# Kernel optimization log

Measured on AMD Instinct MI355X. Metric: run time of the kernel, lower is better.

## Reference

```python
import jax, jax.numpy as jnp
import numpy as np

DIM = 512
H = 48
W = 48
WS = 6
NH = 16
HEAD = DIM // NH
SCALE = HEAD ** -0.5
MLP_RATIO = 4
EPS = 1e-3  # keras LayerNormalization default epsilon
B = 16
L = H * W
M = WS * WS
NW = (H // WS) * (W // WS)


def _rel_pos_index(ws):
    # replicates tf.meshgrid (indexing='xy') construction exactly
    ch = np.arange(ws)
    cw = np.arange(ws)
    coords = np.stack(np.meshgrid(ch, cw))              # (2, ws, ws)
    cf = coords.reshape(2, -1)                          # (2, M)
    cf1 = np.concatenate([cf, np.zeros((2, 1), cf.dtype)], axis=1)  # (2, M+1) with global (0,0)
    rel = cf[:, :, None] - cf1[:, None, :]              # (2, M, M+1)
    rel = rel.transpose(1, 2, 0).copy()
    rel[:, :, 0] += ws - 1
    rel[:, :, 1] += ws - 1
    rel[:, :, 0] *= 2 * ws - 1
    return rel.sum(-1)                                  # (M, M+1)

REL_IDX = jnp.asarray(_rel_pos_index(WS))


def layernorm(x, g, b):
    m = x.mean(-1, keepdims=True)
    v = ((x - m) ** 2).mean(-1, keepdims=True)
    return (x - m) / jnp.sqrt(v + EPS) * g + b


def setup_inputs() -> dict:
    key = jax.random.key(0)
    ks = jax.random.split(key, 8)
    dense = lambda k, i, o: jax.random.normal(k, (i, o), jnp.float32) * (1.0 / np.sqrt(i))
    return dict(
        x=jax.random.normal(ks[0], (B, L, DIM), jnp.float32),
        xavg=jax.random.normal(ks[1], (B, 1, DIM), jnp.float32),
        w_kv=dense(ks[2], DIM, 2 * DIM), b_kv=jnp.zeros((2 * DIM,), jnp.float32),
        w_q=dense(ks[3], DIM, DIM), b_q=jnp.zeros((DIM,), jnp.float32),
        rel_bias_table=jax.random.normal(ks[4], ((2 * WS - 1) ** 2, NH), jnp.float32) * 0.02,
        g1=jnp.ones((DIM,), jnp.float32), be1=jnp.zeros((DIM,), jnp.float32),
        g2=jnp.ones((DIM,), jnp.float32), be2=jnp.zeros((DIM,), jnp.float32),
        w_fc1=dense(ks[5], DIM, MLP_RATIO * DIM), b_fc1=jnp.zeros((MLP_RATIO * DIM,), jnp.float32),
        w_fc2=dense(ks[6], MLP_RATIO * DIM, DIM), b_fc2=jnp.zeros((DIM,), jnp.float32),
    )


def _heads(t):
    # (B*, N, C) -> (B*, NH, N, HEAD)
    return t.reshape(t.shape[0], t.shape[1], NH, HEAD).transpose(0, 2, 1, 3)


def _forward(x, xavg, w_kv, b_kv, w_q, b_q, rel_bias_table, g1, be1, g2, be2,
             w_fc1, b_fc1, w_fc2, b_fc2):
    shortcut, shortcut_avg = x, xavg
    xn = layernorm(x, g1, be1)                          # (B, L, C)
    xavgn = layernorm(xavg, g1, be1)                    # (B, 1, C)

    # window partition: (B, L, C) -> (B*NW, M, C)
    xw = xn.reshape(B, H // WS, WS, W // WS, WS, DIM)
    xw = xw.transpose(0, 1, 3, 2, 4, 5).reshape(B * NW, M, DIM)

    # per-window tokens + repeated global token as keys/values
    xavgR = jnp.repeat(xavgn, NW, axis=0)               # (B*NW, 1, C), batch-major like tf.repeat
    x_c = jnp.concatenate([xw, xavgR], axis=1)          # (B*NW, M+1, C)

    kv = x_c @ w_kv + b_kv                              # (B*NW, M+1, 2C)
    q = xw @ w_q + b_q                                  # (B*NW, M, C)
    q_avg = xavgn @ w_q + b_q                           # (B, 1, C)
    kv_g = xn @ w_kv + b_kv                             # (B, L, 2C)

    k, v = jnp.split(kv, 2, axis=-1)
    kg, vg = jnp.split(kv_g, 2, axis=-1)

    qh = _heads(q) * SCALE                              # (B*NW, NH, M, HEAD)
    attn = jnp.einsum('bhqd,bhkd->bhqk', qh, _heads(k))  # (B*NW, NH, M, M+1)
    bias = rel_bias_table[REL_IDX.reshape(-1)].reshape(M, M + 1, NH)
    attn = attn + bias.transpose(2, 0, 1)[None]
    attn = jax.nn.softmax(attn, axis=-1)
    xo = jnp.einsum('bhqk,bhkd->bhqd', attn, _heads(v))
    xo = xo.transpose(0, 2, 1, 3).reshape(B * NW, M, DIM)

    # global token attends to all tokens
    qg = _heads(q_avg) * SCALE                          # (B, NH, 1, HEAD)
    attng = jax.nn.softmax(jnp.einsum('bhqd,bhkd->bhqk', qg, _heads(kg)), axis=-1)
    xavg_o = jnp.einsum('bhqk,bhkd->bhqd', attng, _heads(vg))
    xavg_o = xavg_o.transpose(0, 2, 1, 3).reshape(B, 1, DIM)

    # window reverse: (B*NW, M, C) -> (B, L, C)
    xr = xo.reshape(B, H // WS, W // WS, WS, WS, DIM)
    xr = xr.transpose(0, 1, 3, 2, 4, 5).reshape(B, L, DIM)

    x = shortcut + xr
    xavg = shortcut_avg + xavg_o

    mlp = lambda t: jax.nn.gelu(t @ w_fc1 + b_fc1, approximate=False) @ w_fc2 + b_fc2
    x = x + mlp(layernorm(x, g2, be2))
    xavg = xavg + mlp(layernorm(xavg, g2, be2))
    return x, xavg


def reference(x, xavg, w_kv, b_kv, w_q, b_q, rel_bias_table, g1, be1, g2, be2,
              w_fc1, b_fc1, w_fc2, b_fc2):
    return _forward(x, xavg, w_kv, b_kv, w_q, b_q, rel_bias_table, g1, be1, g2, be2,
                    w_fc1, b_fc1, w_fc2, b_fc2)
```

## Files before the change

kernel.cpp:

```cpp
#include <hip/hip_runtime.h>
#include <stdint.h>

#define DIM 512
#define NHEAD 16
#define HEADD 32
#define BATCH 16
#define SEQL 2304
#define XROWS (BATCH*SEQL)
#define NROWS (XROWS + BATCH)
#define ATT_SCALE 0.17677669529663687f

typedef __attribute__((ext_vector_type(8))) short short8;
typedef __attribute__((ext_vector_type(4))) float f32x4;

__device__ __forceinline__ float bf2f(unsigned short v) {
    union { unsigned u; float f; } t; t.u = ((unsigned)v) << 16; return t.f;
}
__device__ __forceinline__ unsigned short f2bf(float f) {
    union { float f; unsigned u; } t; t.f = f;
    unsigned r = t.u + 0x7fffu + ((t.u >> 16) & 1u);
    return (unsigned short)(r >> 16);
}
__device__ __forceinline__ void unpack8(const int4 c, float* o) {
    union { unsigned u; float f; } t;
    unsigned w0 = (unsigned)c.x, w1 = (unsigned)c.y, w2 = (unsigned)c.z, w3 = (unsigned)c.w;
    t.u = w0 << 16;         o[0] = t.f;
    t.u = w0 & 0xffff0000u; o[1] = t.f;
    t.u = w1 << 16;         o[2] = t.f;
    t.u = w1 & 0xffff0000u; o[3] = t.f;
    t.u = w2 << 16;         o[4] = t.f;
    t.u = w2 & 0xffff0000u; o[5] = t.f;
    t.u = w3 << 16;         o[6] = t.f;
    t.u = w3 & 0xffff0000u; o[7] = t.f;
}
__device__ __forceinline__ void gl_lds16(const void* g, void* l) {
    __builtin_amdgcn_global_load_lds((const __attribute__((address_space(1))) unsigned int*)g,
                                     (__attribute__((address_space(3))) unsigned int*)l,
                                     16, 0, 0);
}

__device__ __forceinline__ float gelu_exact(float v) {
    union { float f; unsigned u; } zc; zc.f = v * 0.70710678118654752f;
    unsigned sgn = zc.u & 0x80000000u;
    union { float f; unsigned u; } az; az.u = zc.u & 0x7fffffffu;
    float t  = __builtin_amdgcn_rcpf(fmaf(0.3275911f, az.f, 1.0f));
    float p  = t * fmaf(t, fmaf(t, fmaf(t, fmaf(t, 1.061405429f, -1.453152027f),
                                        1.421413741f), -0.284496736f), 0.254829592f);
    float e  = __expf(-az.f * az.f);
    union { float f; unsigned u; } er; er.f = fmaf(-p, e, 1.0f);
    er.u |= sgn;
    return 0.5f * v * (1.0f + er.f);
}

__device__ __forceinline__ void ln_row(const float* __restrict__ src, int lane,
                                       const float* __restrict__ g, const float* __restrict__ be,
                                       unsigned short* __restrict__ outrow) {
    int c0 = lane * 8;
    float4 v0 = *(const float4*)(src + c0);
    float4 v1 = *(const float4*)(src + c0 + 4);
    float s = v0.x+v0.y+v0.z+v0.w + v1.x+v1.y+v1.z+v1.w;
    float q = v0.x*v0.x+v0.y*v0.y+v0.z*v0.z+v0.w*v0.w + v1.x*v1.x+v1.y*v1.y+v1.z*v1.z+v1.w*v1.w;
    for (int m = 1; m < 64; m <<= 1) { s += __shfl_xor(s, m); q += __shfl_xor(q, m); }
    float mean = s * (1.0f/512.0f);
    float var  = q * (1.0f/512.0f) - mean*mean;
    float rs = rsqrtf(var + 1e-3f);
    float4 g0 = *(const float4*)(g + c0);
    float4 g1 = *(const float4*)(g + c0 + 4);
    float4 b0 = *(const float4*)(be + c0);
    float4 b1 = *(const float4*)(be + c0 + 4);
    unsigned short o[8];
    o[0] = f2bf((v0.x-mean)*rs*g0.x + b0.x);
    o[1] = f2bf((v0.y-mean)*rs*g0.y + b0.y);
    o[2] = f2bf((v0.z-mean)*rs*g0.z + b0.z);
    o[3] = f2bf((v0.w-mean)*rs*g0.w + b0.w);
    o[4] = f2bf((v1.x-mean)*rs*g1.x + b1.x);
    o[5] = f2bf((v1.y-mean)*rs*g1.y + b1.y);
    o[6] = f2bf((v1.z-mean)*rs*g1.z + b1.z);
    o[7] = f2bf((v1.w-mean)*rs*g1.w + b1.w);
    *(int4*)(outrow + c0) = *(const int4*)o;
}

#define TPOSE_BLKS 2816
#define SPACK_BLKS 90
#define LN1_BLKS   9220
__global__ __launch_bounds__(256) void prep_kernel(const float* __restrict__ w_q,
                                                   const float* __restrict__ w_kv,
                                                   const float* __restrict__ w_fc1,
                                                   const float* __restrict__ w_fc2,
                                                   unsigned short* __restrict__ Wqkv_t,
                                                   unsigned short* __restrict__ Wfc1_t,
                                                   unsigned short* __restrict__ Wfc2_t,
                                                   const float* __restrict__ b_q,
                                                   const float* __restrict__ b_kv,
                                                   const float* __restrict__ rel_table,
                                                   float* __restrict__ bqkv,
                                                   float* __restrict__ bias_exp,
                                                   const float* __restrict__ x,
                                                   const float* __restrict__ xavg,
                                                   const float* __restrict__ g1,
                                                   const float* __restrict__ be1,
                                                   unsigned short* __restrict__ xn) {
    __shared__ float tile[32][33];
    int blk = blockIdx.x;
    if (blk < TPOSE_BLKS) {
        int t = blk;
        const float* src; unsigned short* dst;
        int Kd, Nd, rowOff, tk;
        if (t < 256)        { src = w_q;   dst = Wqkv_t; Kd = 512;  Nd = 512;  rowOff = 0;   tk = 16; }
        else if (t < 768)   { t -= 256;  src = w_kv;  dst = Wqkv_t; Kd = 512;  Nd = 1024; rowOff = 512; tk = 16; }
        else if (t < 1792)  { t -= 768;  src = w_fc1; dst = Wfc1_t; Kd = 512;  Nd = 2048; rowOff = 0;   tk = 16; }
        else                { t -= 1792; src = w_fc2; dst = Wfc2_t; Kd = 2048; Nd = 512;  rowOff = 0;   tk = 64; }
        int k0 = (t % tk) * 32;
        int n0 = (t / tk) * 32;
        int tx = threadIdx.x & 31, ty = threadIdx.x >> 5;
        #pragma unroll
        for (int r = 0; r < 32; r += 8)
            tile[r + ty][tx] = src[(long)(k0 + r + ty) * Nd + n0 + tx];
        __syncthreads();
        #pragma unroll
        for (int r = 0; r < 32; r += 8)
            dst[(long)(rowOff + n0 + r + ty) * Kd + k0 + tx] = f2bf(tile[tx][r + ty]);
        return;
    }
    blk -= TPOSE_BLKS;
    if (blk < SPACK_BLKS) {
        int i = blk * 256 + threadIdx.x;
        if (i < 1536) { bqkv[i] = (i < 512) ? b_q[i] : b_kv[i - 512]; return; }
        i -= 1536;
        if (i < NHEAD*36*37) {
            int h = i / (36*37); int rem = i % (36*37); int qi = rem / 37; int j = rem % 37;
            int c0m = qi % 6, c1m = qi / 6;
            int c0n = (j < 36) ? (j % 6) : 0;
            int c1n = (j < 36) ? (j / 6) : 0;
            int id = (c0m - c0n + 5) * 11 + (c1m - c1n + 5);
            bias_exp[i] = rel_table[id * NHEAD + h];
        }
        return;
    }
    blk -= SPACK_BLKS;
    int wv = threadIdx.x >> 6, lane = threadIdx.x & 63;
    int r = blk * 4 + wv;
    if (r >= NROWS) return;
    const float* src = (r < XROWS) ? (x + (long)r * DIM) : (xavg + (long)(r - XROWS) * DIM);
    ln_row(src, lane, g1, be1, xn + (long)r * DIM);
}

__global__ __launch_bounds__(256) void ln_kernel(const float* __restrict__ p1,
                                                 const float* __restrict__ g, const float* __restrict__ be,
                                                 unsigned short* __restrict__ out, int nrows) {
    int wv = threadIdx.x >> 6, lane = threadIdx.x & 63;
    int r = blockIdx.x * 4 + wv;
    if (r >= nrows) return;
    ln_row(p1 + (long)r * DIM, lane, g, be, out + (long)r * DIM);
}

template<bool GELU_ACT, bool OUT_BF16, bool HAS_RES>
__global__ __launch_bounds__(256) void gemm_kernel(const short* __restrict__ A,
                                                   const short* __restrict__ Bt,
                                                   const float* __restrict__ bias,
                                                   void* __restrict__ Cout,
                                                   const float* __restrict__ Res,
                                                   int M, int N, int K, int nbx) {
    __shared__ short lds_a[128 * 64];
    __shared__ short lds_b[128 * 64];
    const int tid = threadIdx.x;
    const int lane = tid & 63;
    const int wv = tid >> 6;

    const int nwg = gridDim.x;
    const int orig = blockIdx.x;
    const int q = nwg >> 3, r = nwg & 7;
    const int xcd = orig & 7, lid = orig >> 3;
    const int wg = (xcd < r ? xcd * (q + 1) : r * (q + 1) + (xcd - r) * q) + lid;
    const int m0 = (wg / nbx) * 128;
    const int n0 = (wg % nbx) * 128;
    const int wm = (wv >> 1) * 64;
    const int wn = (wv & 1) * 64;

    f32x4 acc[4][4];
    #pragma unroll
    for (int i = 0; i < 4; i++)
        #pragma unroll
        for (int j = 0; j < 4; j++) { acc[i][j][0]=0.f; acc[i][j][1]=0.f; acc[i][j][2]=0.f; acc[i][j][3]=0.f; }

    const int srow = tid >> 3;
    const int msl  = (tid & 7) ^ (srow & 7);
    const short* Aa = A + (long)(m0 + srow) * K + msl * 8;
    const short* Bb = Bt + (long)(n0 + srow) * K + msl * 8;
    short* la = lds_a + tid * 8;
    short* lb = lds_b + tid * 8;

    const int quad = lane >> 4;
    const int l15 = lane & 15;
    const short* ra0 = lds_a + (wm + l15) * 64 + ((quad)     ^ (l15 & 7)) * 8;
    const short* ra1 = lds_a + (wm + l15) * 64 + ((4 + quad) ^ (l15 & 7)) * 8;
    const short* rb0 = lds_b + (wn + l15) * 64 + ((quad)     ^ (l15 & 7)) * 8;
    const short* rb1 = lds_b + (wn + l15) * 64 + ((4 + quad) ^ (l15 & 7)) * 8;

    for (int k0 = 0; k0 < K; k0 += 64) {
        __syncthreads();
        #pragma unroll
        for (int i = 0; i < 4; i++) {
            gl_lds16(Aa + (long)(i * 32) * K + k0, la + i * 256 * 8);
            gl_lds16(Bb + (long)(i * 32) * K + k0, lb + i * 256 * 8);
        }
        __syncthreads();
        short8 af[4], bf4[4];
        #pragma unroll
        for (int mt = 0; mt < 4; mt++) af[mt] = *(const short8*)(ra0 + mt * 16 * 64);
        #pragma unroll
        for (int nt = 0; nt < 4; nt++) bf4[nt] = *(const short8*)(rb0 + nt * 16 * 64);
        #pragma unroll
        for (int mt = 0; mt < 4; mt++)
            #pragma unroll
            for (int nt = 0; nt < 4; nt++)
                acc[mt][nt] = __builtin_amdgcn_mfma_f32_16x16x32_bf16(af[mt], bf4[nt], acc[mt][nt], 0, 0, 0);
        #pragma unroll
        for (int mt = 0; mt < 4; mt++) af[mt] = *(const short8*)(ra1 + mt * 16 * 64);
        #pragma unroll
        for (int nt = 0; nt < 4; nt++) bf4[nt] = *(const short8*)(rb1 + nt * 16 * 64);
        #pragma unroll
        for (int mt = 0; mt < 4; mt++)
            #pragma unroll
            for (int nt = 0; nt < 4; nt++)
                acc[mt][nt] = __builtin_amdgcn_mfma_f32_16x16x32_bf16(af[mt], bf4[nt], acc[mt][nt], 0, 0, 0);
    }

    #pragma unroll
    for (int mt = 0; mt < 4; mt++) {
        int rbase = m0 + wm + mt * 16 + quad * 4;
        #pragma unroll
        for (int nt = 0; nt < 4; nt++) {
            int col = n0 + wn + nt * 16 + l15;
            float bv = bias[col];
            #pragma unroll
            for (int r2 = 0; r2 < 4; r2++) {
                int row = rbase + r2;
                if (row < M) {
                    float v = acc[mt][nt][r2] + bv;
                    if (GELU_ACT) v = gelu_exact(v);
                    if (HAS_RES) v += Res[(long)row * N + col];
                    if (OUT_BF16) ((unsigned short*)Cout)[(long)row * N + col] = f2bf(v);
                    else          ((float*)Cout)[(long)row * N + col] = v;
                }
            }
        }
    }
}

__global__ __launch_bounds__(256) void attn_kernel(const short* __restrict__ qkv,
                                                   const float* __restrict__ bias_exp,
                                                   const float* __restrict__ xin,
                                                   const float* __restrict__ xavg,
                                                   float* __restrict__ XALL) {
    __shared__ float kvs[4][37 * 64];
    const int tid = threadIdx.x;
    if (blockIdx.x < 4096) {
        const int wv = tid >> 6;
        const int lane = tid & 63;
        const int gw = blockIdx.x * 4 + wv;
        const int win = gw >> 4;
        const int h = gw & 15;
        const int b = win >> 6;
        const int i1 = (win >> 3) & 7;
        const int i3 = win & 7;

        float* lws = kvs[wv];

        for (int c = lane; c < 296; c += 64) {
            int cc = c;
            int voff = 512;
            int doff = 0;
            if (cc >= 148) { cc -= 148; voff = 1024; doff = 32; }
            int row = cc >> 2;
            int part = cc & 3;
            int grow;
            if (row < 36) { int i2 = row / 6, i4 = row % 6; grow = b * SEQL + (i1*6 + i2) * 48 + i3*6 + i4; }
            else grow = XROWS + b;
            int4 raw = *(const int4*)(qkv + (long)grow * 1536 + voff + h * 32 + part * 8);
            float tmp[8];
            unpack8(raw, tmp);
            float* dstp = &lws[row * 64 + doff + part * 8];
            *(float4*)dstp       = make_float4(tmp[0], tmp[1], tmp[2], tmp[3]);
            *(float4*)(dstp + 4) = make_float4(tmp[4], tmp[5], tmp[6], tmp[7]);
        }
        __syncthreads();

        const int qi = lane;
        if (qi >= 36) return;
        int i2 = qi / 6, i4 = qi % 6;
        const int growq = b * SEQL + (i1*6 + i2) * 48 + i3*6 + i4;

        float qr[32];
        {
            const int4* qp = (const int4*)(qkv + (long)growq * 1536 + h * 32);
            unpack8(qp[0], qr); unpack8(qp[1], qr + 8); unpack8(qp[2], qr + 16); unpack8(qp[3], qr + 24);
            #pragma unroll
            for (int d = 0; d < 32; d++) qr[d] *= ATT_SCALE;
        }

        const float* brow = bias_exp + h * (36*37) + qi * 37;
        float s[37];
        float mx = -1e30f;
        #pragma unroll
        for (int j = 0; j < 37; j++) {
            float kr[32];
            #pragma unroll
            for (int t4 = 0; t4 < 8; t4++) *(float4*)(kr + t4*4) = *(const float4*)(lws + j * 64 + t4 * 4);
            float d0 = 0.f, d1 = 0.f, d2 = 0.f, d3 = 0.f;
            #pragma unroll
            for (int dd = 0; dd < 8; dd++) {
                d0 += qr[dd]      * kr[dd];
                d1 += qr[8 + dd]  * kr[8 + dd];
                d2 += qr[16 + dd] * kr[16 + dd];
                d3 += qr[24 + dd] * kr[24 + dd];
            }
            float sv = (d0 + d1 + d2 + d3) + brow[j];
            s[j] = sv;
            mx = fmaxf(mx, sv);
        }
        float sum = 0.f;
        #pragma unroll
        for (int j = 0; j < 37; j++) { s[j] = __expf(s[j] - mx); sum += s[j]; }
        float inv_sum = 1.0f / sum;

        float o[32];
        #pragma unroll
        for (int dd = 0; dd < 32; dd++) o[dd] = 0.f;
        #pragma unroll
        for (int j = 0; j < 37; j++) {
            float vr[32];
            #pragma unroll
            for (int t4 = 0; t4 < 8; t4++) *(float4*)(vr + t4*4) = *(const float4*)(lws + j * 64 + 32 + t4 * 4);
            float p = s[j];
            #pragma unroll
            for (int dd = 0; dd < 32; dd++) o[dd] += p * vr[dd];
        }

        const float* xi = xin + (long)growq * DIM + h * 32;
        float* xo = XALL + (long)growq * DIM + h * 32;
        #pragma unroll
        for (int v4 = 0; v4 < 8; v4++) {
            float4 xv = *(const float4*)(xi + v4 * 4);
            float4 ov;
            ov.x = xv.x + o[v4*4 + 0] * inv_sum;
            ov.y = xv.y + o[v4*4 + 1] * inv_sum;
            ov.z = xv.z + o[v4*4 + 2] * inv_sum;
            ov.w = xv.w + o[v4*4 + 3] * inv_sum;
            *(float4*)(xo + v4 * 4) = ov;
        }
        return;
    }
    {
        const int bb = blockIdx.x - 4096;
        const int b = bb >> 4;
        const int h = bb & 15;
        __shared__ float qs[32];
        __shared__ float redm[4], redsum[4];
        __shared__ float wout[4][32];
        if (tid < 32) qs[tid] = bf2f(((const unsigned short*)qkv)[(long)(XROWS + b) * 1536 + h * 32 + tid]);
        __syncthreads();
        float qr[32];
        #pragma unroll
        for (int d = 0; d < 32; d++) qr[d] = qs[d];
        float s[9];
        float mx = -1e30f;
        #pragma unroll
        for (int i = 0; i < 9; i++) {
            int t = tid + i * 256;
            const int4* kp = (const int4*)(qkv + (long)(b * SEQL + t) * 1536 + 512 + h * 32);
            float kr[32];
            unpack8(kp[0], kr); unpack8(kp[1], kr + 8); unpack8(kp[2], kr + 16); unpack8(kp[3], kr + 24);
            float d0 = 0.f, d1 = 0.f, d2 = 0.f, d3 = 0.f;
            #pragma unroll
            for (int dd = 0; dd < 8; dd++) {
                d0 += qr[dd] * kr[dd]; d1 += qr[8+dd] * kr[8+dd];
                d2 += qr[16+dd] * kr[16+dd]; d3 += qr[24+dd] * kr[24+dd];
            }
            s[i] = (d0 + d1 + d2 + d3) * ATT_SCALE;
            mx = fmaxf(mx, s[i]);
        }
        for (int m = 1; m < 64; m <<= 1) mx = fmaxf(mx, __shfl_xor(mx, m));
        if ((tid & 63) == 0) redm[tid >> 6] = mx;
        __syncthreads();
        mx = fmaxf(fmaxf(redm[0], redm[1]), fmaxf(redm[2], redm[3]));
        float sum = 0.f;
        #pragma unroll
        for (int i = 0; i < 9; i++) { s[i] = __expf(s[i] - mx); sum += s[i]; }
        for (int m = 1; m < 64; m <<= 1) sum += __shfl_xor(sum, m);
        if ((tid & 63) == 0) redsum[tid >> 6] = sum;
        __syncthreads();
        sum = redsum[0] + redsum[1] + redsum[2] + redsum[3];
        float o[32];
        #pragma unroll
        for (int d = 0; d < 32; d++) o[d] = 0.f;
        #pragma unroll
        for (int i = 0; i < 9; i++) {
            int t = tid + i * 256;
            const int4* vp = (const int4*)(qkv + (long)(b * SEQL + t) * 1536 + 1024 + h * 32);
            float vr[32];
            unpack8(vp[0], vr); unpack8(vp[1], vr + 8); unpack8(vp[2], vr + 16); unpack8(vp[3], vr + 24);
            float p = s[i];
            #pragma unroll
            for (int d = 0; d < 32; d++) o[d] += p * vr[d];
        }
        for (int m = 1; m < 64; m <<= 1) {
            #pragma unroll
            for (int d = 0; d < 32; d++) o[d] += __shfl_xor(o[d], m);
        }
        if ((tid & 63) == 0) {
            #pragma unroll
            for (int d = 0; d < 32; d++) wout[tid >> 6][d] = o[d];
        }
        __syncthreads();
        if (tid < 32) {
            float t = wout[0][tid] + wout[1][tid] + wout[2][tid] + wout[3][tid];
            XALL[(long)(XROWS + b) * DIM + h * 32 + tid] = xavg[b * DIM + h * 32 + tid] + t / sum;
        }
    }
}

extern "C" void kernel_launch(void* const* d_in, const int* in_sizes, int n_in,
                              void* d_out, int out_size, void* d_ws, size_t ws_size,
                              hipStream_t stream) {
    const float* x      = (const float*)d_in[0];
    const float* xavg   = (const float*)d_in[1];
    const float* w_kv   = (const float*)d_in[2];
    const float* b_kv   = (const float*)d_in[3];
    const float* w_q    = (const float*)d_in[4];
    const float* b_q    = (const float*)d_in[5];
    const float* rel    = (const float*)d_in[6];
    const float* g1     = (const float*)d_in[7];
    const float* be1    = (const float*)d_in[8];
    const float* g2     = (const float*)d_in[9];
    const float* be2    = (const float*)d_in[10];
    const float* w_fc1  = (const float*)d_in[11];
    const float* b_fc1  = (const float*)d_in[12];
    const float* w_fc2  = (const float*)d_in[13];
    const float* b_fc2  = (const float*)d_in[14];

    char* ws = (char*)d_ws;
    size_t off = 0;
    auto alloc = [&](size_t bytes) { void* p = ws + off; off += (bytes + 255) & ~(size_t)255; return p; };
    short* qkv_h          = (short*)alloc((size_t)NROWS * 2048 * 2);
    float* XALL           = (float*)alloc((size_t)NROWS * 512 * 4);
    short* xn             = (short*)alloc((size_t)NROWS * 512 * 2);
    unsigned short* Wqkv_t = (unsigned short*)alloc((size_t)1536 * 512 * 2);
    unsigned short* Wfc1_t = (unsigned short*)alloc((size_t)2048 * 512 * 2);
    unsigned short* Wfc2_t = (unsigned short*)alloc((size_t)512 * 2048 * 2);
    float* bqkv           = (float*)alloc(1536 * 4);
    float* bias_exp       = (float*)alloc((size_t)NHEAD * 36 * 37 * 4);

    const int MB = (NROWS + 127) / 128;

    prep_kernel<<<TPOSE_BLKS + SPACK_BLKS + LN1_BLKS, 256, 0, stream>>>(
        w_q, w_kv, w_fc1, w_fc2, Wqkv_t, Wfc1_t, Wfc2_t,
        b_q, b_kv, rel, bqkv, bias_exp,
        x, xavg, g1, be1, (unsigned short*)xn);
    gemm_kernel<false, true, false><<<12 * MB, 256, 0, stream>>>(
        xn, (const short*)Wqkv_t, bqkv, qkv_h, nullptr, NROWS, 1536, 512, 12);
    attn_kernel<<<4096 + 256, 256, 0, stream>>>(qkv_h, bias_exp, x, xavg, XALL);
    ln_kernel<<<(NROWS + 3) / 4, 256, 0, stream>>>(XALL, g2, be2, (unsigned short*)xn, NROWS);
    gemm_kernel<true, true, false><<<16 * MB, 256, 0, stream>>>(
        xn, (const short*)Wfc1_t, b_fc1, qkv_h, nullptr, NROWS, 2048, 512, 16);
    gemm_kernel<false, false, true><<<4 * MB, 256, 0, stream>>>(
        qkv_h, (const short*)Wfc2_t, b_fc2, d_out, XALL, NROWS, 512, 2048, 4);
}
```

Baseline: 720.4 us.

## Add 256x256 double-buffered MFMA GEMM for QKV and fc1 projections

Adds a new 512-thread GEMM kernel with 256x256 output tiles and a double-buffered LDS pipeline fed by direct global-to-LDS loads over K-steps of 32. It replaces the 128-tile GEMM for the QKV and fc1 projections; fc2 keeps the old kernel. The larger tiles raise arithmetic intensity and cut redundant global reads. Prefetching the next K-slice while the current one runs through MFMA is meant to hide load latency. In exchange it uses 128 accumulator registers per thread, more LDS per block and fewer blocks per wave, and its epilogue does scalar, partly strided stores.

```diff
diff --git a/kernel.cpp b/kernel.cpp
--- a/kernel.cpp
+++ b/kernel.cpp
@@ -154,6 +154,100 @@
     ln_row(p1 + (long)r * DIM, lane, g, be, out + (long)r * DIM);
 }
 
+template<bool GELU_ACT, bool OUT_BF16>
+__global__ __launch_bounds__(512) void gemm256_kernel(const short* __restrict__ A,
+                                                      const short* __restrict__ Bt,
+                                                      const float* __restrict__ bias,
+                                                      void* __restrict__ Cout,
+                                                      int M, int N, int K, int nbx) {
+    __shared__ short lds_a[2][256 * 32];
+    __shared__ short lds_b[2][256 * 32];
+    const int tid = threadIdx.x;
+    const int lane = tid & 63;
+    const int wv = tid >> 6;
+
+    const int nwg = gridDim.x;
+    const int orig = blockIdx.x;
+    const int q = nwg >> 3, r = nwg & 7;
+    const int xcd = orig & 7, lid = orig >> 3;
+    const int wg = (xcd < r ? xcd * (q + 1) : r * (q + 1) + (xcd - r) * q) + lid;
+    const int m0 = (wg / nbx) * 256;
+    const int n0 = (wg % nbx) * 256;
+    const int wm = (wv >> 2) * 128;
+    const int wn = (wv & 3) * 64;
+
+    f32x4 acc[8][4];
+    #pragma unroll
+    for (int i = 0; i < 8; i++)
+        #pragma unroll
+        for (int j = 0; j < 4; j++) { acc[i][j][0]=0.f; acc[i][j][1]=0.f; acc[i][j][2]=0.f; acc[i][j][3]=0.f; }
+
+    const int su   = (tid & 7) ^ ((tid >> 3) & 7);
+    const int srow = 2 * (tid >> 3) + (su >> 2);
+    const int ssl  = su & 3;
+    const short* Aa = A + (long)(m0 + srow) * K + ssl * 8;
+    const short* Bb = Bt + (long)(n0 + srow) * K + ssl * 8;
+
+    const int quad = lane >> 4;
+    const int l15 = lane & 15;
+    const int la0 = (wm >> 1) + (l15 >> 1);
+    const int ro_a = (la0 * 8 + ((((l15 & 1) << 2) | quad) ^ (l15 >> 1))) * 8;
+    const int lb0 = (wn >> 1) + (l15 >> 1);
+    const int ro_b = (lb0 * 8 + ((((l15 & 1) << 2) | quad) ^ (l15 >> 1))) * 8;
+
+    auto stage = [&](int buf, int k0) {
+        short* la = &lds_a[buf][tid * 8];
+        short* lb = &lds_b[buf][tid * 8];
+        #pragma unroll
+        for (int i = 0; i < 2; i++) {
+            gl_lds16(Aa + (long)(i * 128) * K + k0, la + i * 4096);
+            gl_lds16(Bb + (long)(i * 128) * K + k0, lb + i * 4096);
+        }
+    };
+
+    stage(0, 0);
+    __syncthreads();
+    int cur = 0;
+    const int NT = K >> 5;
+    for (int kt = 0; kt < NT; ++kt) {
+        if (kt + 1 < NT) stage(cur ^ 1, (kt + 1) << 5);
+        const short* ba = lds_a[cur];
+        const short* bb = lds_b[cur];
+        short8 af[8], bf4[4];
+        #pragma unroll
+        for (int mt = 0; mt < 8; mt++) af[mt] = *(const short8*)(ba + ro_a + mt * 512);
+        #pragma unroll
+        for (int nt = 0; nt < 4; nt++) bf4[nt] = *(const short8*)(bb + ro_b + nt * 512);
+        #pragma unroll
+        for (int mt = 0; mt < 8; mt++)
+            #pragma unroll
+            for (int nt = 0; nt < 4; nt++)
+                acc[mt][nt] = __builtin_amdgcn_mfma_f32_16x16x32_bf16(af[mt], bf4[nt], acc[mt][nt], 0, 0, 0);
+        __syncthreads();
+        cur ^= 1;
+    }
+
+    #pragma unroll
+    for (int mt = 0; mt < 8; mt++) {
+        int rbase = m0 + wm + mt * 16 + quad * 4;
+        #pragma unroll
+        for (int nt = 0; nt < 4; nt++) {
+            int col = n0 + wn + nt * 16 + l15;
+            float bv = bias[col];
+            #pragma unroll
+            for (int r2 = 0; r2 < 4; r2++) {
+                int row = rbase + r2;
+                if (row < M) {
+                    float v = acc[mt][nt][r2] + bv;
+                    if (GELU_ACT) v = gelu_exact(v);
+                    if (OUT_BF16) ((unsigned short*)Cout)[(long)row * N + col] = f2bf(v);
+                    else          ((float*)Cout)[(long)row * N + col] = v;
+                }
+            }
+        }
+    }
+}
+
 template<bool GELU_ACT, bool OUT_BF16, bool HAS_RES>
 __global__ __launch_bounds__(256) void gemm_kernel(const short* __restrict__ A,
                                                    const short* __restrict__ Bt,
@@ -451,18 +545,19 @@
     float* bqkv           = (float*)alloc(1536 * 4);
     float* bias_exp       = (float*)alloc((size_t)NHEAD * 36 * 37 * 4);
 
-    const int MB = (NROWS + 127) / 128;
+    const int MB128 = (NROWS + 127) / 128;
+    const int MB256 = (NROWS + 255) / 256;
 
     prep_kernel<<<TPOSE_BLKS + SPACK_BLKS + LN1_BLKS, 256, 0, stream>>>(
         w_q, w_kv, w_fc1, w_fc2, Wqkv_t, Wfc1_t, Wfc2_t,
         b_q, b_kv, rel, bqkv, bias_exp,
         x, xavg, g1, be1, (unsigned short*)xn);
-    gemm_kernel<false, true, false><<<12 * MB, 256, 0, stream>>>(
-        xn, (const short*)Wqkv_t, bqkv, qkv_h, nullptr, NROWS, 1536, 512, 12);
+    gemm256_kernel<false, true><<<6 * MB256, 512, 0, stream>>>(
+        xn, (const short*)Wqkv_t, bqkv, qkv_h, NROWS, 1536, 512, 6);
     attn_kernel<<<4096 + 256, 256, 0, stream>>>(qkv_h, bias_exp, x, xavg, XALL);
     ln_kernel<<<(NROWS + 3) / 4, 256, 0, stream>>>(XALL, g2, be2, (unsigned short*)xn, NROWS);
-    gemm_kernel<true, true, false><<<16 * MB, 256, 0, stream>>>(
-        xn, (const short*)Wfc1_t, b_fc1, qkv_h, nullptr, NROWS, 2048, 512, 16);
-    gemm_kernel<false, false, true><<<4 * MB, 256, 0, stream>>>(
+    gemm256_kernel<true, true><<<8 * MB256, 512, 0, stream>>>(
+        xn, (const short*)Wfc1_t, b_fc1, qkv_h, NROWS, 2048, 512, 8);
+    gemm_kernel<false, false, true><<<4 * MB128, 256, 0, stream>>>(
         qkv_h, (const short*)Wfc2_t, b_fc2, d_out, XALL, NROWS, 512, 2048, 4);
 }
```

Result: slower. 779.2 us (+8.2%).

## Compute windowed attention QK^T and PV with bf16 MFMA instructions

Applied to the files above, without the earlier changes.

Replaces the per-lane scalar FP32 dot-product attention (one query per lane, with K/V staged as float in LDS) with MFMA 16x16x32 bf16 tiles for both QK^T and P·V. V is staged transposed in LDS, probabilities are rounded to bf16 and written to LDS, and the softmax uses cross-lane shuffles, with padding to 48 rows/cols. The aim is to cut the FP32 FMA and LDS traffic of the attention kernel, which is only one part of the whole pipeline. In exchange it rounds P to bf16 and adds LDS staging, zero-fill and a sync.

```diff
diff --git a/kernel.cpp b/kernel.cpp
--- a/kernel.cpp
+++ b/kernel.cpp
@@ -253,7 +253,9 @@
                                                    const float* __restrict__ xin,
                                                    const float* __restrict__ xavg,
                                                    float* __restrict__ XALL) {
-    __shared__ float kvs[4][37 * 64];
+    __shared__ short vt[4][32 * 64];
+    __shared__ short pl[4][48 * 64];
+    __shared__ float sums[4][48];
     const int tid = threadIdx.x;
     if (blockIdx.x < 4096) {
         const int wv = tid >> 6;
@@ -264,90 +266,142 @@
         const int b = win >> 6;
         const int i1 = (win >> 3) & 7;
         const int i3 = win & 7;
-
-        float* lws = kvs[wv];
-
-        for (int c = lane; c < 296; c += 64) {
-            int cc = c;
-            int voff = 512;
-            int doff = 0;
-            if (cc >= 148) { cc -= 148; voff = 1024; doff = 32; }
-            int row = cc >> 2;
-            int part = cc & 3;
-            int grow;
-            if (row < 36) { int i2 = row / 6, i4 = row % 6; grow = b * SEQL + (i1*6 + i2) * 48 + i3*6 + i4; }
+        short* VT = vt[wv];
+        short* PL = pl[wv];
+        float* SM = sums[wv];
+        const int quad = lane >> 4;
+        const int l15 = lane & 15;
+
+        {
+            int4 z; z.x = 0; z.y = 0; z.z = 0; z.w = 0;
+            int4* v4 = (int4*)VT;
+            #pragma unroll
+            for (int i = 0; i < 4; i++) v4[lane + 64 * i] = z;
+            int4* p4 = (int4*)PL;
+            #pragma unroll
+            for (int i = 0; i < 6; i++) p4[lane + 64 * i] = z;
+        }
+        for (int c = lane; c < 148; c += 64) {
+            int j = c >> 2, dg = c & 3;
+            long grow;
+            if (j < 36) { int i2 = j / 6, i4 = j % 6; grow = (long)b * SEQL + (i1*6 + i2) * 48 + i3*6 + i4; }
             else grow = XROWS + b;
-            int4 raw = *(const int4*)(qkv + (long)grow * 1536 + voff + h * 32 + part * 8);
-            float tmp[8];
-            unpack8(raw, tmp);
-            float* dstp = &lws[row * 64 + doff + part * 8];
-            *(float4*)dstp       = make_float4(tmp[0], tmp[1], tmp[2], tmp[3]);
-            *(float4*)(dstp + 4) = make_float4(tmp[4], tmp[5], tmp[6], tmp[7]);
-        }
-        __syncthreads();
-
-        const int qi = lane;
-        if (qi >= 36) return;
-        int i2 = qi / 6, i4 = qi % 6;
-        const int growq = b * SEQL + (i1*6 + i2) * 48 + i3*6 + i4;
-
-        float qr[32];
-        {
-            const int4* qp = (const int4*)(qkv + (long)growq * 1536 + h * 32);
-            unpack8(qp[0], qr); unpack8(qp[1], qr + 8); unpack8(qp[2], qr + 16); unpack8(qp[3], qr + 24);
-            #pragma unroll
-            for (int d = 0; d < 32; d++) qr[d] *= ATT_SCALE;
-        }
-
-        const float* brow = bias_exp + h * (36*37) + qi * 37;
-        float s[37];
-        float mx = -1e30f;
-        #pragma unroll
-        for (int j = 0; j < 37; j++) {
-            float kr[32];
-            #pragma unroll
-            for (int t4 = 0; t4 < 8; t4++) *(float4*)(kr + t4*4) = *(const float4*)(lws + j * 64 + t4 * 4);
-            float d0 = 0.f, d1 = 0.f, d2 = 0.f, d3 = 0.f;
-            #pragma unroll
-            for (int dd = 0; dd < 8; dd++) {
-                d0 += qr[dd]      * kr[dd];
-                d1 += qr[8 + dd]  * kr[8 + dd];
-                d2 += qr[16 + dd] * kr[16 + dd];
-                d3 += qr[24 + dd] * kr[24 + dd];
-            }
-            float sv = (d0 + d1 + d2 + d3) + brow[j];
-            s[j] = sv;
-            mx = fmaxf(mx, sv);
-        }
-        float sum = 0.f;
-        #pragma unroll
-        for (int j = 0; j < 37; j++) { s[j] = __expf(s[j] - mx); sum += s[j]; }
-        float inv_sum = 1.0f / sum;
-
-        float o[32];
-        #pragma unroll
-        for (int dd = 0; dd < 32; dd++) o[dd] = 0.f;
-        #pragma unroll
-        for (int j = 0; j < 37; j++) {
-            float vr[32];
-            #pragma unroll
-            for (int t4 = 0; t4 < 8; t4++) *(float4*)(vr + t4*4) = *(const float4*)(lws + j * 64 + 32 + t4 * 4);
-            float p = s[j];
-            #pragma unroll
-            for (int dd = 0; dd < 32; dd++) o[dd] += p * vr[dd];
-        }
-
-        const float* xi = xin + (long)growq * DIM + h * 32;
-        float* xo = XALL + (long)growq * DIM + h * 32;
-        #pragma unroll
-        for (int v4 = 0; v4 < 8; v4++) {
-            float4 xv = *(const float4*)(xi + v4 * 4);
-            float4 ov;
-            ov.x = xv.x + o[v4*4 + 0] * inv_sum;
-            ov.y = xv.y + o[v4*4 + 1] * inv_sum;
-            ov.z = xv.z + o[v4*4 + 2] * inv_sum;
-            ov.w = xv.w + o[v4*4 + 3] * inv_sum;
-            *(float4*)(xo + v4 * 4) = ov;
+            int4 raw = *(const int4*)(qkv + grow * 1536 + 1024 + h * 32 + dg * 8);
+            const unsigned short* u = (const unsigned short*)&raw;
+            #pragma unroll
+            for (int t = 0; t < 8; t++) VT[(dg * 8 + t) * 64 + j] = (short)u[t];
+        }
+        __syncthreads();
+
+        short8 qf[3], kf[3];
+        #pragma unroll
+        for (int tm = 0; tm < 3; tm++) {
+            int qi = tm * 16 + l15;
+            if (qi < 36) {
+                int i2 = qi / 6, i4 = qi % 6;
+                long grow = (long)b * SEQL + (i1*6 + i2) * 48 + i3*6 + i4;
+                qf[tm] = *(const short8*)(qkv + grow * 1536 + h * 32 + quad * 8);
+            } else {
+                #pragma unroll
+                for (int i = 0; i < 8; i++) qf[tm][i] = 0;
+            }
+        }
+        #pragma unroll
+        for (int tn = 0; tn < 3; tn++) {
+            int j = tn * 16 + l15;
+            if (j <= 36) {
+                long grow;
+                if (j < 36) { int i2 = j / 6, i4 = j % 6; grow = (long)b * SEQL + (i1*6 + i2) * 48 + i3*6 + i4; }
+                else grow = XROWS + b;
+                kf[tn] = *(const short8*)(qkv + grow * 1536 + 512 + h * 32 + quad * 8);
+            } else {
+                #pragma unroll
+                for (int i = 0; i < 8; i++) kf[tn][i] = 0;
+            }
+        }
+        f32x4 s[3][3];
+        #pragma unroll
+        for (int tm = 0; tm < 3; tm++)
+            #pragma unroll
+            for (int tn = 0; tn < 3; tn++) {
+                f32x4 z; z[0]=0.f; z[1]=0.f; z[2]=0.f; z[3]=0.f;
+                s[tm][tn] = __builtin_amdgcn_mfma_f32_16x16x32_bf16(qf[tm], kf[tn], z, 0, 0, 0);
+            }
+        #pragma unroll
+        for (int tm = 0; tm < 3; tm++)
+            #pragma unroll
+            for (int r = 0; r < 4; r++) {
+                int qi = tm * 16 + quad * 4 + r;
+                const float* bh = bias_exp + h * (36*37) + (qi < 36 ? qi : 35) * 37;
+                #pragma unroll
+                for (int tn = 0; tn < 3; tn++) {
+                    int j = tn * 16 + l15;
+                    float bv = bh[j <= 36 ? j : 36];
+                    float v = fmaf(s[tm][tn][r], ATT_SCALE, bv);
+                    s[tm][tn][r] = (j <= 36) ? v : -1e30f;
+                }
+            }
+        #pragma unroll
+        for (int tm = 0; tm < 3; tm++)
+            #pragma unroll
+            for (int r = 0; r < 4; r++) {
+                float mx = fmaxf(fmaxf(s[tm][0][r], s[tm][1][r]), s[tm][2][r]);
+                for (int m = 1; m < 16; m <<= 1) mx = fmaxf(mx, __shfl_xor(mx, m));
+                float e0 = __expf(s[tm][0][r] - mx);
+                float e1 = __expf(s[tm][1][r] - mx);
+                float e2 = __expf(s[tm][2][r] - mx);
+                float sum = e0 + e1 + e2;
+                for (int m = 1; m < 16; m <<= 1) sum += __shfl_xor(sum, m);
+                s[tm][0][r] = e0; s[tm][1][r] = e1; s[tm][2][r] = e2;
+                if (l15 == 0) SM[tm * 16 + quad * 4 + r] = 1.0f / sum;
+            }
+        #pragma unroll
+        for (int tm = 0; tm < 3; tm++)
+            #pragma unroll
+            for (int r = 0; r < 4; r++) {
+                int row = (tm * 16 + quad * 4 + r) * 64;
+                #pragma unroll
+                for (int tn = 0; tn < 3; tn++)
+                    PL[row + tn * 16 + l15] = (short)f2bf(s[tm][tn][r]);
+            }
+        f32x4 o[2][3];
+        #pragma unroll
+        for (int i = 0; i < 2; i++)
+            #pragma unroll
+            for (int j = 0; j < 3; j++) { o[i][j][0]=0.f; o[i][j][1]=0.f; o[i][j][2]=0.f; o[i][j][3]=0.f; }
+        #pragma unroll
+        for (int ch = 0; ch < 2; ch++) {
+            short8 va[2], pb[3];
+            #pragma unroll
+            for (int tmd = 0; tmd < 2; tmd++)
+                va[tmd] = *(const short8*)(VT + (tmd * 16 + l15) * 64 + ch * 32 + quad * 8);
+            #pragma unroll
+            for (int tnq = 0; tnq < 3; tnq++)
+                pb[tnq] = *(const short8*)(PL + (tnq * 16 + l15) * 64 + ch * 32 + quad * 8);
+            #pragma unroll
+            for (int tmd = 0; tmd < 2; tmd++)
+                #pragma unroll
+                for (int tnq = 0; tnq < 3; tnq++)
+                    o[tmd][tnq] = __builtin_amdgcn_mfma_f32_16x16x32_bf16(va[tmd], pb[tnq], o[tmd][tnq], 0, 0, 0);
+        }
+        #pragma unroll
+        for (int tnq = 0; tnq < 3; tnq++) {
+            int qi = tnq * 16 + l15;
+            if (qi >= 36) continue;
+            int i2 = qi / 6, i4 = qi % 6;
+            long growq = (long)b * SEQL + (i1*6 + i2) * 48 + i3*6 + i4;
+            float is = SM[qi];
+            #pragma unroll
+            for (int tmd = 0; tmd < 2; tmd++) {
+                long base = growq * DIM + h * 32 + tmd * 16 + quad * 4;
+                float4 xv = *(const float4*)(xin + base);
+                float4 ov;
+                ov.x = xv.x + o[tmd][tnq][0] * is;
+                ov.y = xv.y + o[tmd][tnq][1] * is;
+                ov.z = xv.z + o[tmd][tnq][2] * is;
+                ov.w = xv.w + o[tmd][tnq][3] * is;
+                *(float4*)(XALL + base) = ov;
+            }
         }
         return;
     }
```

New measurement: 679.6 us. 1.06x faster.
